# Performance work log

Hardware: AMD Instinct MI355X
Metric: run time of the kernel (lower is better)

## Reference

```python
import jax, jax.numpy as jnp
import numpy as np

DIM = 384
HEADS = 6
K = 10          # default k of DynamicGraphAttention
HID = 1536      # int(dim * mlp_ratio)
LN_EPS = 1e-5


def layernorm(x, g, b):
    m = jnp.mean(x, -1, keepdims=True)
    var = jnp.mean((x - m) ** 2, -1, keepdims=True)
    return (x - m) * jax.lax.rsqrt(var + LN_EPS) * g + b


def setup_inputs() -> dict:
    key = jax.random.key(0)
    ks = jax.random.split(key, 12)
    B, N, M, C = 16, 1024, 512, DIM
    s = 0.02
    return dict(
        q=jax.random.normal(ks[0], (B, N, C), jnp.float32),
        v=jax.random.normal(ks[1], (B, M, C), jnp.float32),
        q_pos=jax.random.normal(ks[2], (B, N, 3), jnp.float32),
        v_pos=jax.random.normal(ks[3], (B, M, 3), jnp.float32),
        norm1_g=jnp.ones((C,), jnp.float32), norm1_b=jnp.zeros((C,), jnp.float32),
        qkv_w=jax.random.normal(ks[4], (C, 3 * C), jnp.float32) * s,  # qkv_bias=False
        proj_w=jax.random.normal(ks[5], (C, C), jnp.float32) * s,
        proj_b=jnp.zeros((C,), jnp.float32),
        normq_g=jnp.ones((C,), jnp.float32), normq_b=jnp.zeros((C,), jnp.float32),
        normv_g=jnp.ones((C,), jnp.float32), normv_b=jnp.zeros((C,), jnp.float32),
        knn_w=jax.random.normal(ks[6], (2 * C, C), jnp.float32) * s,
        knn_b=jnp.zeros((C,), jnp.float32),
        norm2_g=jnp.ones((C,), jnp.float32), norm2_b=jnp.zeros((C,), jnp.float32),
        fc1_w=jax.random.normal(ks[7], (C, HID), jnp.float32) * s,
        fc1_b=jnp.zeros((HID,), jnp.float32),
        fc2_w=jax.random.normal(ks[8], (HID, C), jnp.float32) * s,
        fc2_b=jnp.zeros((C,), jnp.float32),
    )


def reference(q, v, q_pos, v_pos,
              norm1_g, norm1_b, qkv_w, proj_w, proj_b,
              normq_g, normq_b, normv_g, normv_b, knn_w, knn_b,
              norm2_g, norm2_b, fc1_w, fc1_b, fc2_w, fc2_b):
    B, N, C = q.shape
    D = C // HEADS

    # --- multi-head self-attention with pre-norm residual ---
    x = layernorm(q, norm1_g, norm1_b)
    qkv = (x @ qkv_w).reshape(B, N, 3, HEADS, D)
    qh, kh, vh = qkv[:, :, 0], qkv[:, :, 1], qkv[:, :, 2]   # [B,N,H,D]
    attn = jnp.einsum('bnhd,bmhd->bhnm', qh, kh) * (D ** -0.5)
    attn = jax.nn.softmax(attn, axis=-1)
    sa = jnp.einsum('bhnm,bmhd->bnhd', attn, vh).reshape(B, N, C)
    sa = sa @ proj_w + proj_b
    q = q + sa

    # --- dynamic graph cross-attention (knn gather + diff-concat MLP + max) ---
    nq = layernorm(q, normq_g, normq_b)          # [B,N,C]
    nv = layernorm(v, normv_g, normv_b)          # [B,M,C]
    # squared distances between query and kv positions: [B,N,M]
    d = (jnp.sum(q_pos ** 2, -1)[:, :, None]
         + jnp.sum(v_pos ** 2, -1)[:, None, :]
         - 2.0 * jnp.einsum('bnc,bmc->bnm', q_pos, v_pos))
    _, idx = jax.lax.top_k(-d, K)                # K nearest neighbors, [B,N,K]
    local_v = jax.vmap(lambda vv, ii: vv[ii])(nv, idx)   # [B,N,K,C]
    qe = nq[:, :, None, :]                                # [B,N,1,C]
    feat = jnp.concatenate(
        [local_v - qe, jnp.broadcast_to(qe, local_v.shape)], axis=-1)  # [B,N,K,2C]
    g = jax.nn.leaky_relu(feat @ knn_w + knn_b, negative_slope=0.2)
    q = q + jnp.max(g, axis=-2)                  # max over K neighbors

    # --- MLP with pre-norm residual ---
    h = layernorm(q, norm2_g, norm2_b)
    h = jax.nn.gelu(h @ fc1_w + fc1_b, approximate=False)
    h = h @ fc2_w + fc2_b
    return q + h
```

## Files before the change

### kernel.cpp

```cpp
#include <hip/hip_runtime.h>
#include <hip/hip_bf16.h>

#define CDIM 384
#define NHEAD 6
#define DHEAD 64
#define BB 16
#define NQ 1024
#define MV 512
#define HIDD 1536
#define KNN 10

typedef __attribute__((ext_vector_type(8))) __bf16 bf16x8;
typedef __attribute__((ext_vector_type(4))) float f32x4;
typedef __attribute__((ext_vector_type(4))) short short4v;

__global__ void cast_all_kernel(const float* __restrict__ qkv_w, const float* __restrict__ proj_w,
                                const float* __restrict__ knn_w, const float* __restrict__ fc1_w,
                                const float* __restrict__ fc2_w,
                                __hip_bfloat16* __restrict__ Wqkv_t,
                                __hip_bfloat16* __restrict__ Wproj_t,
                                __hip_bfloat16* __restrict__ W1_t,
                                __hip_bfloat16* __restrict__ Wd_t,
                                __hip_bfloat16* __restrict__ Wfc1_t,
                                __hip_bfloat16* __restrict__ Wfc2_t) {
  __shared__ float t1[32][33];
  __shared__ float t2[32][33];
  int gid = blockIdx.x;
  int tx = threadIdx.x, ty = threadIdx.y;
  if (gid >= 576 && gid < 720) {
    int id = gid - 576;
    int k0 = (id % 12) * 32, n0 = (id / 12) * 32;
#pragma unroll
    for (int i = 0; i < 4; i++) {
      int k = k0 + ty + i * 8;
      float w1 = knn_w[(size_t)k * CDIM + n0 + tx];
      float w2 = knn_w[(size_t)(CDIM + k) * CDIM + n0 + tx];
      t1[ty + i * 8][tx] = w1;
      t2[ty + i * 8][tx] = w2 - w1;
    }
    __syncthreads();
#pragma unroll
    for (int i = 0; i < 4; i++) {
      W1_t[(size_t)(n0 + ty + i * 8) * CDIM + k0 + tx] = __float2bfloat16(t1[tx][ty + i * 8]);
      Wd_t[(size_t)(n0 + ty + i * 8) * CDIM + k0 + tx] = __float2bfloat16(t2[tx][ty + i * 8]);
    }
    return;
  }
  const float* W;
  __hip_bfloat16* Wt;
  int Kd, Nd, k0, n0;
  if (gid < 432) {
    W = qkv_w; Wt = Wqkv_t; Kd = 384; Nd = 1152;
    k0 = (gid % 12) * 32; n0 = (gid / 12) * 32;
  } else if (gid < 576) {
    int id = gid - 432;
    W = proj_w; Wt = Wproj_t; Kd = 384; Nd = 384;
    k0 = (id % 12) * 32; n0 = (id / 12) * 32;
  } else if (gid < 1296) {
    int id = gid - 720;
    W = fc1_w; Wt = Wfc1_t; Kd = 384; Nd = 1536;
    k0 = (id % 12) * 32; n0 = (id / 12) * 32;
  } else {
    int id = gid - 1296;
    W = fc2_w; Wt = Wfc2_t; Kd = 1536; Nd = 384;
    k0 = (id % 48) * 32; n0 = (id / 48) * 32;
  }
#pragma unroll
  for (int i = 0; i < 4; i++)
    t1[ty + i * 8][tx] = W[(size_t)(k0 + ty + i * 8) * Nd + n0 + tx];
  __syncthreads();
#pragma unroll
  for (int i = 0; i < 4; i++)
    Wt[(size_t)(n0 + ty + i * 8) * Kd + k0 + tx] = __float2bfloat16(t1[tx][ty + i * 8]);
}

__device__ inline void ln_row(const float* __restrict__ xr, const float* __restrict__ gw,
                              const float* __restrict__ bw, __hip_bfloat16* __restrict__ outr,
                              int lane) {
  float v0[6];
  float s = 0.f;
#pragma unroll
  for (int i = 0; i < 3; i++) {
    float2 t = *reinterpret_cast<const float2*>(xr + i * 128 + lane * 2);
    v0[i * 2] = t.x; v0[i * 2 + 1] = t.y; s += t.x + t.y;
  }
  for (int off = 32; off; off >>= 1) s += __shfl_xor(s, off);
  float mean = s * (1.f / 384.f);
  float sq = 0.f;
#pragma unroll
  for (int i = 0; i < 6; i++) { float d = v0[i] - mean; sq += d * d; }
  for (int off = 32; off; off >>= 1) sq += __shfl_xor(sq, off);
  float rstd = rsqrtf(sq * (1.f / 384.f) + 1e-5f);
#pragma unroll
  for (int i = 0; i < 3; i++) {
    int c = i * 128 + lane * 2;
    float2 gg = *reinterpret_cast<const float2*>(gw + c);
    float2 bb = *reinterpret_cast<const float2*>(bw + c);
    __hip_bfloat162 p;
    p.x = __float2bfloat16((v0[i * 2] - mean) * rstd * gg.x + bb.x);
    p.y = __float2bfloat16((v0[i * 2 + 1] - mean) * rstd * gg.y + bb.y);
    *reinterpret_cast<__hip_bfloat162*>(outr + c) = p;
  }
}

__global__ __launch_bounds__(256) void ln_kernel(const float* __restrict__ x,
                                                 const float* __restrict__ gw,
                                                 const float* __restrict__ bw,
                                                 __hip_bfloat16* __restrict__ out, int rows) {
  int wave = (int)((blockIdx.x * blockDim.x + threadIdx.x) >> 6);
  int lane = threadIdx.x & 63;
  if (wave >= rows) return;
  ln_row(x + (size_t)wave * CDIM, gw, bw, out + (size_t)wave * CDIM, lane);
}

__global__ __launch_bounds__(256) void ln_dual_kernel(const float* __restrict__ q1,
                                                      const float* __restrict__ v,
                                                      const float* __restrict__ gq,
                                                      const float* __restrict__ bq,
                                                      const float* __restrict__ gv,
                                                      const float* __restrict__ bv,
                                                      __hip_bfloat16* __restrict__ Xbf,
                                                      __hip_bfloat16* __restrict__ NV) {
  int wave = (int)((blockIdx.x * blockDim.x + threadIdx.x) >> 6);
  int lane = threadIdx.x & 63;
  if (wave < BB * NQ) {
    ln_row(q1 + (size_t)wave * CDIM, gq, bq, Xbf + (size_t)wave * CDIM, lane);
  } else {
    int r = wave - BB * NQ;
    ln_row(v + (size_t)r * CDIM, gv, bv, NV + (size_t)r * CDIM, lane);
  }
}

template <int EPI>
__global__ __launch_bounds__(256) void gemm_kernel(const __hip_bfloat16* __restrict__ A,
                                                   const __hip_bfloat16* __restrict__ Bt,
                                                   const float* __restrict__ bias,
                                                   const float* __restrict__ resid,
                                                   void* __restrict__ outp,
                                                   void* __restrict__ out2,
                                                   void* __restrict__ out3,
                                                   int M, int N, int Kdim) {
  __shared__ __align__(16) __hip_bfloat16 As[128 * 64];
  __shared__ __align__(16) __hip_bfloat16 Bs[128 * 64];
  int m0 = blockIdx.y * 128, n0 = blockIdx.x * 128;
  int t = threadIdx.x;
  int lane = t & 63, w = t >> 6;
  int wrow = w >> 1, wcol = w & 1;
  int lg = lane >> 4, lr = lane & 15;
  int gcol = (((lane & 7) ^ (lane >> 3)) * 8);
  const __hip_bfloat16* Ab = A + (size_t)(m0 + w * 8 + (lane >> 3)) * Kdim + gcol;
  const __hip_bfloat16* Bb = Bt + (size_t)(n0 + w * 8 + (lane >> 3)) * Kdim + gcol;
  char* AsB = (char*)As;
  char* BsB = (char*)Bs;
  f32x4 acc[4][4] = {};
  for (int k0 = 0; k0 < Kdim; k0 += 64) {
    if (k0) __syncthreads();
#pragma unroll
    for (int i = 0; i < 4; i++)
      __builtin_amdgcn_global_load_lds(
          (const __attribute__((address_space(1))) void*)(Ab + (size_t)(i * 32) * Kdim + k0),
          (__attribute__((address_space(3))) void*)(AsB + (i * 4 + w) * 1024), 16, 0, 0);
#pragma unroll
    for (int i = 0; i < 4; i++)
      __builtin_amdgcn_global_load_lds(
          (const __attribute__((address_space(1))) void*)(Bb + (size_t)(i * 32) * Kdim + k0),
          (__attribute__((address_space(3))) void*)(BsB + (i * 4 + w) * 1024), 16, 0, 0);
    __syncthreads();
#pragma unroll
    for (int kk = 0; kk < 2; kk++) {
      bf16x8 a[4], b[4];
#pragma unroll
      for (int i = 0; i < 4; i++) {
        int ra = wrow * 64 + i * 16 + lr;
        int rb = wcol * 64 + i * 16 + lr;
        int sw = (((kk << 2) | lg) ^ (lr & 7)) * 16;
        a[i] = *reinterpret_cast<const bf16x8*>(AsB + ra * 128 + sw);
        b[i] = *reinterpret_cast<const bf16x8*>(BsB + rb * 128 + sw);
      }
#pragma unroll
      for (int i = 0; i < 4; i++)
#pragma unroll
        for (int j = 0; j < 4; j++)
          acc[i][j] = __builtin_amdgcn_mfma_f32_16x16x32_bf16(a[i], b[j], acc[i][j], 0, 0, 0);
    }
  }
#pragma unroll
  for (int i = 0; i < 4; i++)
#pragma unroll
    for (int j = 0; j < 4; j++) {
      int col = n0 + wcol * 64 + j * 16 + lr;
#pragma unroll
      for (int r = 0; r < 4; r++) {
        int row = m0 + wrow * 64 + i * 16 + lg * 4 + r;
        float v = acc[i][j][r];
        if (EPI == 5) {
          int b = row >> 10, n = row & 1023;
          if (col < CDIM) {
            int h = col >> 6, d = col & 63;
            ((__hip_bfloat16*)outp)[(((size_t)(b * NHEAD + h)) * NQ + n) * DHEAD + d] =
                __float2bfloat16(v * 0.18033688f);
          } else if (col < 2 * CDIM) {
            int c = col - CDIM, h = c >> 6, d = c & 63;
            ((__hip_bfloat16*)out2)[(((size_t)(b * NHEAD + h)) * NQ + n) * DHEAD + d] =
                __float2bfloat16(v);
          } else {
            int c = col - 2 * CDIM, h = c >> 6, d = c & 63;
            ((__hip_bfloat16*)out3)[(((size_t)(b * NHEAD + h)) * DHEAD + d) * NQ + n] =
                __float2bfloat16(v);
          }
        } else {
          if (EPI == 1 || EPI == 2 || EPI == 3) v += bias[col];
          if (EPI == 2) v += resid[(size_t)row * N + col];
          if (EPI == 3) v = 0.5f * v * (1.f + erff(v * 0.70710678118654752f));
          if (EPI == 0 || EPI == 3)
            ((__hip_bfloat16*)outp)[(size_t)row * N + col] = __float2bfloat16(v);
          else
            ((float*)outp)[(size_t)row * N + col] = v;
        }
      }
    }
}

__global__ __launch_bounds__(256) void attn_kernel(const __hip_bfloat16* __restrict__ Qb,
                                                   const __hip_bfloat16* __restrict__ Kb,
                                                   const __hip_bfloat16* __restrict__ Vt,
                                                   __hip_bfloat16* __restrict__ SAb) {
  __shared__ __align__(16) __hip_bfloat16 Ks[2][64][72];
  __shared__ __align__(16) __hip_bfloat16 Vs[2][64][72];
  int bh = blockIdx.x % 96;
  int qblk = blockIdx.x / 96;
  int t = threadIdx.x;
  int w = t >> 6, lane = t & 63;
  int lg = lane >> 4, lr = lane & 15;
  const __hip_bfloat16* Qp = Qb + (size_t)bh * NQ * DHEAD;
  const __hip_bfloat16* Kp = Kb + (size_t)bh * NQ * DHEAD;
  const __hip_bfloat16* Vp = Vt + (size_t)bh * DHEAD * NQ;
  int q0 = qblk * 128 + w * 32;
  bf16x8 qf[2][2];
#pragma unroll
  for (int qt = 0; qt < 2; qt++)
#pragma unroll
    for (int kk = 0; kk < 2; kk++)
      qf[qt][kk] = *reinterpret_cast<const bf16x8*>(
          Qp + (size_t)(q0 + qt * 16 + lr) * DHEAD + kk * 32 + lg * 8);
  int srow = w * 16 + (lane >> 2);
  int scol = (lane & 3) * 16;
  uint4 kr0 = *reinterpret_cast<const uint4*>(Kp + (size_t)srow * DHEAD + scol);
  uint4 kr1 = *reinterpret_cast<const uint4*>(Kp + (size_t)srow * DHEAD + scol + 8);
  uint4 vr0 = *reinterpret_cast<const uint4*>(Vp + (size_t)srow * NQ + scol);
  uint4 vr1 = *reinterpret_cast<const uint4*>(Vp + (size_t)srow * NQ + scol + 8);
  *reinterpret_cast<uint4*>(&Ks[0][srow][scol]) = kr0;
  *reinterpret_cast<uint4*>(&Ks[0][srow][scol + 8]) = kr1;
  *reinterpret_cast<uint4*>(&Vs[0][srow][scol]) = vr0;
  *reinterpret_cast<uint4*>(&Vs[0][srow][scol + 8]) = vr1;
  f32x4 o[2][4] = {};
  float m_[2] = {-1e30f, -1e30f};
  float l_[2] = {0.f, 0.f};
  __syncthreads();
  for (int kt = 0; kt < 16; kt++) {
    int cur = kt & 1;
    if (kt < 15) {
      int kb = (kt + 1) * 64;
      kr0 = *reinterpret_cast<const uint4*>(Kp + (size_t)(kb + srow) * DHEAD + scol);
      kr1 = *reinterpret_cast<const uint4*>(Kp + (size_t)(kb + srow) * DHEAD + scol + 8);
      vr0 = *reinterpret_cast<const uint4*>(Vp + (size_t)srow * NQ + kb + scol);
      vr1 = *reinterpret_cast<const uint4*>(Vp + (size_t)srow * NQ + kb + scol + 8);
    }
    f32x4 s[4][2] = {};
#pragma unroll
    for (int kti = 0; kti < 4; kti++)
#pragma unroll
      for (int kk = 0; kk < 2; kk++) {
        bf16x8 a = *reinterpret_cast<const bf16x8*>(&Ks[cur][kti * 16 + lr][kk * 32 + lg * 8]);
#pragma unroll
        for (int qt = 0; qt < 2; qt++)
          s[kti][qt] = __builtin_amdgcn_mfma_f32_16x16x32_bf16(a, qf[qt][kk], s[kti][qt], 0, 0, 0);
      }
#pragma unroll
    for (int qt = 0; qt < 2; qt++) {
      float a0 = fmaxf(fmaxf(s[0][qt][0], s[0][qt][1]), fmaxf(s[0][qt][2], s[0][qt][3]));
      float a1 = fmaxf(fmaxf(s[1][qt][0], s[1][qt][1]), fmaxf(s[1][qt][2], s[1][qt][3]));
      float a2 = fmaxf(fmaxf(s[2][qt][0], s[2][qt][1]), fmaxf(s[2][qt][2], s[2][qt][3]));
      float a3 = fmaxf(fmaxf(s[3][qt][0], s[3][qt][1]), fmaxf(s[3][qt][2], s[3][qt][3]));
      float lmax = fmaxf(fmaxf(a0, a1), fmaxf(a2, a3));
      if (!__all(lmax - m_[qt] <= 8.f)) {
        float pmax = fmaxf(lmax, __shfl_xor(lmax, 16));
        pmax = fmaxf(pmax, __shfl_xor(pmax, 32));
        float mn = fmaxf(m_[qt], pmax);
        float corr = __builtin_amdgcn_exp2f(m_[qt] - mn);
        l_[qt] *= corr;
        m_[qt] = mn;
#pragma unroll
        for (int r = 0; r < 4; r++) {
          float cr = __shfl(corr, (lane & 48) | (((lane >> 4) & 3) * 4 + r));
#pragma unroll
          for (int dt = 0; dt < 4; dt++) o[qt][dt][r] *= cr;
        }
      }
      float m = m_[qt];
      float ls = 0.f;
#pragma unroll
      for (int kti = 0; kti < 4; kti++) {
        float p0 = __builtin_amdgcn_exp2f(s[kti][qt][0] - m);
        float p1 = __builtin_amdgcn_exp2f(s[kti][qt][1] - m);
        float p2 = __builtin_amdgcn_exp2f(s[kti][qt][2] - m);
        float p3 = __builtin_amdgcn_exp2f(s[kti][qt][3] - m);
        s[kti][qt][0] = p0; s[kti][qt][1] = p1; s[kti][qt][2] = p2; s[kti][qt][3] = p3;
        ls += (p0 + p1) + (p2 + p3);
      }
      l_[qt] += ls;
    }
#pragma unroll
    for (int kti = 0; kti < 4; kti++) {
      short4v pa[2];
#pragma unroll
      for (int qt = 0; qt < 2; qt++) {
#pragma unroll
        for (int r = 0; r < 4; r++) {
          __bf16 hv = (__bf16)s[kti][qt][r];
          pa[qt][r] = __builtin_bit_cast(short, hv);
        }
      }
#pragma unroll
      for (int dt = 0; dt < 4; dt++) {
        short4v vb = *reinterpret_cast<const short4v*>(&Vs[cur][dt * 16 + lr][kti * 16 + lg * 4]);
#pragma unroll
        for (int qt = 0; qt < 2; qt++)
          o[qt][dt] = __builtin_amdgcn_mfma_f32_16x16x16bf16_1k(pa[qt], vb, o[qt][dt], 0, 0, 0);
      }
    }
    if (kt < 15) {
      int nb = cur ^ 1;
      *reinterpret_cast<uint4*>(&Ks[nb][srow][scol]) = kr0;
      *reinterpret_cast<uint4*>(&Ks[nb][srow][scol + 8]) = kr1;
      *reinterpret_cast<uint4*>(&Vs[nb][srow][scol]) = vr0;
      *reinterpret_cast<uint4*>(&Vs[nb][srow][scol + 8]) = vr1;
      __syncthreads();
    }
  }
#pragma unroll
  for (int qt = 0; qt < 2; qt++) {
    l_[qt] += __shfl_xor(l_[qt], 16);
    l_[qt] += __shfl_xor(l_[qt], 32);
  }
  int b = bh / NHEAD, h = bh % NHEAD;
#pragma unroll
  for (int qt = 0; qt < 2; qt++)
#pragma unroll
    for (int r = 0; r < 4; r++) {
      float li = __shfl(l_[qt], (lane & 48) | (((lane >> 4) & 3) * 4 + r));
      float inv = 1.f / li;
      int row = q0 + qt * 16 + ((lane >> 4) & 3) * 4 + r;
#pragma unroll
      for (int dt = 0; dt < 4; dt++)
        SAb[((size_t)(b * NQ + row)) * CDIM + h * DHEAD + dt * 16 + lr] =
            __float2bfloat16(o[qt][dt][r] * inv);
    }
}

__global__ __launch_bounds__(256) void knn_fused_kernel(const float* __restrict__ q_pos,
                                                        const float* __restrict__ v_pos,
                                                        const float* __restrict__ A1,
                                                        const float* __restrict__ A2,
                                                        const float* __restrict__ q1,
                                                        const float* __restrict__ g2,
                                                        const float* __restrict__ b2,
                                                        float* __restrict__ q2,
                                                        __hip_bfloat16* __restrict__ xout) {
  int wq = (int)((blockIdx.x * blockDim.x + threadIdx.x) >> 6);
  int lane = threadIdx.x & 63;
  if (wq >= BB * NQ) return;
  int b = wq >> 10;
  const float* qp = q_pos + (size_t)wq * 3;
  double qx = qp[0], qy = qp[1], qz = qp[2];
  double qs = qx * qx + qy * qy + qz * qz;
  double dloc[8];
#pragma unroll
  for (int j = 0; j < 8; j++) {
    int m = lane + 64 * j;
    const float* vp = v_pos + ((size_t)b * MV + m) * 3;
    double vx = vp[0], vy = vp[1], vz = vp[2];
    double vs = vx * vx + vy * vy + vz * vz;
    dloc[j] = qs + vs - 2.0 * (qx * vx + qy * vy + qz * vz);
  }
  float a2[6], mx[6];
#pragma unroll
  for (int i = 0; i < 6; i++) {
    a2[i] = A2[(size_t)wq * CDIM + lane + 64 * i];
    mx[i] = -1e30f;
  }
  for (int k = 0; k < KNN; k++) {
    double best = dloc[0];
    int bj = 0;
#pragma unroll
    for (int j = 1; j < 8; j++)
      if (dloc[j] < best) { best = dloc[j]; bj = j; }
    int bm = lane + 64 * bj;
    for (int off = 1; off < 64; off <<= 1) {
      double od = __shfl_xor(best, off);
      int om = __shfl_xor(bm, off);
      if (od < best || (od == best && om < bm)) { best = od; bm = om; }
    }
    const float* a1 = A1 + ((size_t)b * MV + bm) * CDIM;
#pragma unroll
    for (int i = 0; i < 6; i++) {
      float g = a1[lane + 64 * i] + a2[i];
      g = g > 0.f ? g : 0.2f * g;
      mx[i] = fmaxf(mx[i], g);
    }
#pragma unroll
    for (int j = 0; j < 8; j++)
      if (bm == lane + 64 * j) dloc[j] = 1e300;
  }
  float vals[6];
  float s = 0.f;
#pragma unroll
  for (int i = 0; i < 6; i++) {
    vals[i] = q1[(size_t)wq * CDIM + lane + 64 * i] + mx[i];
    s += vals[i];
  }
  for (int off = 32; off; off >>= 1) s += __shfl_xor(s, off);
  float mean = s * (1.f / 384.f);
  float sq = 0.f;
#pragma unroll
  for (int i = 0; i < 6; i++) { float d = vals[i] - mean; sq += d * d; }
  for (int off = 32; off; off >>= 1) sq += __shfl_xor(sq, off);
  float rstd = rsqrtf(sq * (1.f / 384.f) + 1e-5f);
#pragma unroll
  for (int i = 0; i < 6; i++) {
    int c = lane + 64 * i;
    q2[(size_t)wq * CDIM + c] = vals[i];
    xout[(size_t)wq * CDIM + c] = __float2bfloat16((vals[i] - mean) * rstd * g2[c] + b2[c]);
  }
}

extern "C" void kernel_launch(void* const* d_in, const int* in_sizes, int n_in,
                              void* d_out, int out_size, void* d_ws, size_t ws_size,
                              hipStream_t stream) {
  const float* q = (const float*)d_in[0];
  const float* v = (const float*)d_in[1];
  const float* q_pos = (const float*)d_in[2];
  const float* v_pos = (const float*)d_in[3];
  const float* norm1_g = (const float*)d_in[4];
  const float* norm1_b = (const float*)d_in[5];
  const float* qkv_w = (const float*)d_in[6];
  const float* proj_w = (const float*)d_in[7];
  const float* proj_b = (const float*)d_in[8];
  const float* normq_g = (const float*)d_in[9];
  const float* normq_b = (const float*)d_in[10];
  const float* normv_g = (const float*)d_in[11];
  const float* normv_b = (const float*)d_in[12];
  const float* knn_w = (const float*)d_in[13];
  const float* knn_b = (const float*)d_in[14];
  const float* norm2_g = (const float*)d_in[15];
  const float* norm2_b = (const float*)d_in[16];
  const float* fc1_w = (const float*)d_in[17];
  const float* fc1_b = (const float*)d_in[18];
  const float* fc2_w = (const float*)d_in[19];
  const float* fc2_b = (const float*)d_in[20];

  char* ws = (char*)d_ws;
  const size_t SZ_Wqkv = (size_t)1152 * 384 * 2;
  const size_t SZ_W384 = (size_t)384 * 384 * 2;
  const size_t SZ_Wfc = (size_t)1536 * 384 * 2;
  const size_t SZ_Xbf = (size_t)16384 * 384 * 2;
  const size_t SZ_QKV = (size_t)16384 * 1152 * 2;
  const size_t SZ_q32 = (size_t)16384 * 384 * 4;
  const size_t SZ_NV = (size_t)8192 * 384 * 2;

  size_t o_Wqkv = 0;
  size_t o_Wproj = o_Wqkv + SZ_Wqkv;
  size_t o_W1 = o_Wproj + SZ_W384;
  size_t o_Wd = o_W1 + SZ_W384;
  size_t o_Wfc1 = o_Wd + SZ_W384;
  size_t o_Wfc2 = o_Wfc1 + SZ_Wfc;
  size_t o_Xbf = o_Wfc2 + SZ_Wfc;
  size_t o_QKV = o_Xbf + SZ_Xbf;
  size_t o_A1 = o_QKV;
  size_t o_A2 = o_QKV + (size_t)8192 * 384 * 4;
  size_t o_Qb = o_QKV + SZ_QKV;
  size_t o_Kb = o_Qb + SZ_Xbf;
  size_t o_Vt = o_Kb + SZ_Xbf;
  size_t o_SA = o_Vt + SZ_Xbf;
  size_t o_H1 = o_Qb;
  size_t o_q1 = o_SA + SZ_Xbf;
  size_t o_NV = o_q1 + SZ_q32;
  size_t o_q2 = o_NV + SZ_NV;

  __hip_bfloat16* Wqkv_t = (__hip_bfloat16*)(ws + o_Wqkv);
  __hip_bfloat16* Wproj_t = (__hip_bfloat16*)(ws + o_Wproj);
  __hip_bfloat16* W1_t = (__hip_bfloat16*)(ws + o_W1);
  __hip_bfloat16* Wd_t = (__hip_bfloat16*)(ws + o_Wd);
  __hip_bfloat16* Wfc1_t = (__hip_bfloat16*)(ws + o_Wfc1);
  __hip_bfloat16* Wfc2_t = (__hip_bfloat16*)(ws + o_Wfc2);
  __hip_bfloat16* Xbf = (__hip_bfloat16*)(ws + o_Xbf);
  float* A1f = (float*)(ws + o_A1);
  float* A2f = (float*)(ws + o_A2);
  __hip_bfloat16* Qb = (__hip_bfloat16*)(ws + o_Qb);
  __hip_bfloat16* Kb = (__hip_bfloat16*)(ws + o_Kb);
  __hip_bfloat16* Vt = (__hip_bfloat16*)(ws + o_Vt);
  __hip_bfloat16* SAb = (__hip_bfloat16*)(ws + o_SA);
  __hip_bfloat16* H1 = (__hip_bfloat16*)(ws + o_H1);
  float* q1 = (float*)(ws + o_q1);
  __hip_bfloat16* NV = (__hip_bfloat16*)(ws + o_NV);
  float* q2 = (float*)(ws + o_q2);
  float* outf = (float*)d_out;

  cast_all_kernel<<<1872, dim3(32, 8), 0, stream>>>(qkv_w, proj_w, knn_w, fc1_w, fc2_w,
                                                    Wqkv_t, Wproj_t, W1_t, Wd_t, Wfc1_t, Wfc2_t);
  ln_kernel<<<4096, 256, 0, stream>>>(q, norm1_g, norm1_b, Xbf, 16384);
  gemm_kernel<5><<<dim3(9, 128), 256, 0, stream>>>(Xbf, Wqkv_t, nullptr, nullptr,
                                                   Qb, Kb, Vt, 16384, 1152, 384);
  attn_kernel<<<768, 256, 0, stream>>>(Qb, Kb, Vt, SAb);
  gemm_kernel<2><<<dim3(3, 128), 256, 0, stream>>>(SAb, Wproj_t, proj_b, q, q1,
                                                   nullptr, nullptr, 16384, 384, 384);
  ln_dual_kernel<<<6144, 256, 0, stream>>>(q1, v, normq_g, normq_b, normv_g, normv_b, Xbf, NV);
  gemm_kernel<4><<<dim3(3, 64), 256, 0, stream>>>(NV, W1_t, nullptr, nullptr, A1f,
                                                  nullptr, nullptr, 8192, 384, 384);
  gemm_kernel<1><<<dim3(3, 128), 256, 0, stream>>>(Xbf, Wd_t, knn_b, nullptr, A2f,
                                                   nullptr, nullptr, 16384, 384, 384);
  knn_fused_kernel<<<4096, 256, 0, stream>>>(q_pos, v_pos, A1f, A2f, q1,
                                             norm2_g, norm2_b, q2, Xbf);
  gemm_kernel<3><<<dim3(12, 128), 256, 0, stream>>>(Xbf, Wfc1_t, fc1_b, nullptr, H1,
                                                    nullptr, nullptr, 16384, 1536, 384);
  gemm_kernel<2><<<dim3(3, 128), 256, 0, stream>>>(H1, Wfc2_t, fc2_b, q2, outf,
                                                   nullptr, nullptr, 16384, 384, 1536);
}
```

Before: 335.1 us.

## Merge weight cast with LN1, batch KNN GEMMs, use 64-row tiles for N=384 GEMMs

Folds the weight transpose/cast and the first layernorm into one prep kernel, and merges the two KNN projection GEMMs (A1 from NV, A2 from normalized q) into a single launch. The GEMM is templated on M tile size, and the N=384 GEMMs now use 64-row tiles. On a 256-CU part this doubles the block count from 384 to 768, which should fill the GPU better. The trade-off is less A/B reuse per block, and W1_t and Wd_t must sit contiguously in the workspace.

```diff
diff --git a/kernel.cpp b/kernel.cpp
--- a/kernel.cpp
+++ b/kernel.cpp
@@ -14,19 +14,54 @@
 typedef __attribute__((ext_vector_type(4))) float f32x4;
 typedef __attribute__((ext_vector_type(4))) short short4v;
 
-__global__ void cast_all_kernel(const float* __restrict__ qkv_w, const float* __restrict__ proj_w,
-                                const float* __restrict__ knn_w, const float* __restrict__ fc1_w,
-                                const float* __restrict__ fc2_w,
-                                __hip_bfloat16* __restrict__ Wqkv_t,
-                                __hip_bfloat16* __restrict__ Wproj_t,
-                                __hip_bfloat16* __restrict__ W1_t,
-                                __hip_bfloat16* __restrict__ Wd_t,
-                                __hip_bfloat16* __restrict__ Wfc1_t,
-                                __hip_bfloat16* __restrict__ Wfc2_t) {
+__device__ inline void ln_row(const float* __restrict__ xr, const float* __restrict__ gw,
+                              const float* __restrict__ bw, __hip_bfloat16* __restrict__ outr,
+                              int lane) {
+  float v0[6];
+  float s = 0.f;
+#pragma unroll
+  for (int i = 0; i < 3; i++) {
+    float2 t = *reinterpret_cast<const float2*>(xr + i * 128 + lane * 2);
+    v0[i * 2] = t.x; v0[i * 2 + 1] = t.y; s += t.x + t.y;
+  }
+  for (int off = 32; off; off >>= 1) s += __shfl_xor(s, off);
+  float mean = s * (1.f / 384.f);
+  float sq = 0.f;
+#pragma unroll
+  for (int i = 0; i < 6; i++) { float d = v0[i] - mean; sq += d * d; }
+  for (int off = 32; off; off >>= 1) sq += __shfl_xor(sq, off);
+  float rstd = rsqrtf(sq * (1.f / 384.f) + 1e-5f);
+#pragma unroll
+  for (int i = 0; i < 3; i++) {
+    int c = i * 128 + lane * 2;
+    float2 gg = *reinterpret_cast<const float2*>(gw + c);
+    float2 bb = *reinterpret_cast<const float2*>(bw + c);
+    __hip_bfloat162 p;
+    p.x = __float2bfloat16((v0[i * 2] - mean) * rstd * gg.x + bb.x);
+    p.y = __float2bfloat16((v0[i * 2 + 1] - mean) * rstd * gg.y + bb.y);
+    *reinterpret_cast<__hip_bfloat162*>(outr + c) = p;
+  }
+}
+
+__global__ __launch_bounds__(256) void prep_kernel(
+    const float* __restrict__ qkv_w, const float* __restrict__ proj_w,
+    const float* __restrict__ knn_w, const float* __restrict__ fc1_w,
+    const float* __restrict__ fc2_w, const float* __restrict__ q,
+    const float* __restrict__ g1, const float* __restrict__ b1,
+    __hip_bfloat16* __restrict__ Wqkv_t, __hip_bfloat16* __restrict__ Wproj_t,
+    __hip_bfloat16* __restrict__ W1_t, __hip_bfloat16* __restrict__ Wd_t,
+    __hip_bfloat16* __restrict__ Wfc1_t, __hip_bfloat16* __restrict__ Wfc2_t,
+    __hip_bfloat16* __restrict__ Xbf) {
+  int gid = blockIdx.x;
+  if (gid >= 1872) {
+    int wave = (gid - 1872) * 4 + ((int)threadIdx.x >> 6);
+    int lane = threadIdx.x & 63;
+    ln_row(q + (size_t)wave * CDIM, g1, b1, Xbf + (size_t)wave * CDIM, lane);
+    return;
+  }
   __shared__ float t1[32][33];
   __shared__ float t2[32][33];
-  int gid = blockIdx.x;
-  int tx = threadIdx.x, ty = threadIdx.y;
+  int tx = threadIdx.x & 31, ty = (int)threadIdx.x >> 5;
   if (gid >= 576 && gid < 720) {
     int id = gid - 576;
     int k0 = (id % 12) * 32, n0 = (id / 12) * 32;
@@ -74,45 +109,6 @@
     Wt[(size_t)(n0 + ty + i * 8) * Kd + k0 + tx] = __float2bfloat16(t1[tx][ty + i * 8]);
 }
 
-__device__ inline void ln_row(const float* __restrict__ xr, const float* __restrict__ gw,
-                              const float* __restrict__ bw, __hip_bfloat16* __restrict__ outr,
-                              int lane) {
-  float v0[6];
-  float s = 0.f;
-#pragma unroll
-  for (int i = 0; i < 3; i++) {
-    float2 t = *reinterpret_cast<const float2*>(xr + i * 128 + lane * 2);
-    v0[i * 2] = t.x; v0[i * 2 + 1] = t.y; s += t.x + t.y;
-  }
-  for (int off = 32; off; off >>= 1) s += __shfl_xor(s, off);
-  float mean = s * (1.f / 384.f);
-  float sq = 0.f;
-#pragma unroll
-  for (int i = 0; i < 6; i++) { float d = v0[i] - mean; sq += d * d; }
-  for (int off = 32; off; off >>= 1) sq += __shfl_xor(sq, off);
-  float rstd = rsqrtf(sq * (1.f / 384.f) + 1e-5f);
-#pragma unroll
-  for (int i = 0; i < 3; i++) {
-    int c = i * 128 + lane * 2;
-    float2 gg = *reinterpret_cast<const float2*>(gw + c);
-    float2 bb = *reinterpret_cast<const float2*>(bw + c);
-    __hip_bfloat162 p;
-    p.x = __float2bfloat16((v0[i * 2] - mean) * rstd * gg.x + bb.x);
-    p.y = __float2bfloat16((v0[i * 2 + 1] - mean) * rstd * gg.y + bb.y);
-    *reinterpret_cast<__hip_bfloat162*>(outr + c) = p;
-  }
-}
-
-__global__ __launch_bounds__(256) void ln_kernel(const float* __restrict__ x,
-                                                 const float* __restrict__ gw,
-                                                 const float* __restrict__ bw,
-                                                 __hip_bfloat16* __restrict__ out, int rows) {
-  int wave = (int)((blockIdx.x * blockDim.x + threadIdx.x) >> 6);
-  int lane = threadIdx.x & 63;
-  if (wave >= rows) return;
-  ln_row(x + (size_t)wave * CDIM, gw, bw, out + (size_t)wave * CDIM, lane);
-}
-
 __global__ __launch_bounds__(256) void ln_dual_kernel(const float* __restrict__ q1,
                                                       const float* __restrict__ v,
                                                       const float* __restrict__ gq,
@@ -131,7 +127,7 @@
   }
 }
 
-template <int EPI>
+template <int EPI, int BM>
 __global__ __launch_bounds__(256) void gemm_kernel(const __hip_bfloat16* __restrict__ A,
                                                    const __hip_bfloat16* __restrict__ Bt,
                                                    const float* __restrict__ bias,
@@ -140,23 +136,37 @@
                                                    void* __restrict__ out2,
                                                    void* __restrict__ out3,
                                                    int M, int N, int Kdim) {
-  __shared__ __align__(16) __hip_bfloat16 As[128 * 64];
+  constexpr int MI = BM / 32;
+  __shared__ __align__(16) __hip_bfloat16 As[BM * 64];
   __shared__ __align__(16) __hip_bfloat16 Bs[128 * 64];
-  int m0 = blockIdx.y * 128, n0 = blockIdx.x * 128;
+  int m0 = blockIdx.y * BM, n0 = blockIdx.x * 128;
+  const __hip_bfloat16* Ause = A;
+  const __hip_bfloat16* Bt_use = Bt;
+  bool isA1 = false;
+  if (EPI == 6) {
+    constexpr int A2B = 16384 / BM;
+    if ((int)blockIdx.y >= A2B) {
+      isA1 = true;
+      m0 = (blockIdx.y - A2B) * BM;
+      Ause = (const __hip_bfloat16*)out3;
+    } else {
+      Bt_use = Bt + (size_t)384 * 384;
+    }
+  }
   int t = threadIdx.x;
   int lane = t & 63, w = t >> 6;
   int wrow = w >> 1, wcol = w & 1;
   int lg = lane >> 4, lr = lane & 15;
   int gcol = (((lane & 7) ^ (lane >> 3)) * 8);
-  const __hip_bfloat16* Ab = A + (size_t)(m0 + w * 8 + (lane >> 3)) * Kdim + gcol;
-  const __hip_bfloat16* Bb = Bt + (size_t)(n0 + w * 8 + (lane >> 3)) * Kdim + gcol;
+  const __hip_bfloat16* Ab = Ause + (size_t)(m0 + w * 8 + (lane >> 3)) * Kdim + gcol;
+  const __hip_bfloat16* Bb = Bt_use + (size_t)(n0 + w * 8 + (lane >> 3)) * Kdim + gcol;
   char* AsB = (char*)As;
   char* BsB = (char*)Bs;
-  f32x4 acc[4][4] = {};
+  f32x4 acc[MI][4] = {};
   for (int k0 = 0; k0 < Kdim; k0 += 64) {
     if (k0) __syncthreads();
 #pragma unroll
-    for (int i = 0; i < 4; i++)
+    for (int i = 0; i < MI; i++)
       __builtin_amdgcn_global_load_lds(
           (const __attribute__((address_space(1))) void*)(Ab + (size_t)(i * 32) * Kdim + k0),
           (__attribute__((address_space(3))) void*)(AsB + (i * 4 + w) * 1024), 16, 0, 0);
@@ -168,30 +178,34 @@
     __syncthreads();
 #pragma unroll
     for (int kk = 0; kk < 2; kk++) {
-      bf16x8 a[4], b[4];
-#pragma unroll
-      for (int i = 0; i < 4; i++) {
-        int ra = wrow * 64 + i * 16 + lr;
-        int rb = wcol * 64 + i * 16 + lr;
+      bf16x8 a[MI], b[4];
+#pragma unroll
+      for (int i = 0; i < MI; i++) {
+        int ra = wrow * (BM / 2) + i * 16 + lr;
         int sw = (((kk << 2) | lg) ^ (lr & 7)) * 16;
         a[i] = *reinterpret_cast<const bf16x8*>(AsB + ra * 128 + sw);
-        b[i] = *reinterpret_cast<const bf16x8*>(BsB + rb * 128 + sw);
-      }
-#pragma unroll
-      for (int i = 0; i < 4; i++)
+      }
+#pragma unroll
+      for (int j = 0; j < 4; j++) {
+        int rb = wcol * 64 + j * 16 + lr;
+        int sw = (((kk << 2) | lg) ^ (lr & 7)) * 16;
+        b[j] = *reinterpret_cast<const bf16x8*>(BsB + rb * 128 + sw);
+      }
+#pragma unroll
+      for (int i = 0; i < MI; i++)
 #pragma unroll
         for (int j = 0; j < 4; j++)
           acc[i][j] = __builtin_amdgcn_mfma_f32_16x16x32_bf16(a[i], b[j], acc[i][j], 0, 0, 0);
     }
   }
 #pragma unroll
-  for (int i = 0; i < 4; i++)
+  for (int i = 0; i < MI; i++)
 #pragma unroll
     for (int j = 0; j < 4; j++) {
       int col = n0 + wcol * 64 + j * 16 + lr;
 #pragma unroll
       for (int r = 0; r < 4; r++) {
-        int row = m0 + wrow * 64 + i * 16 + lg * 4 + r;
+        int row = m0 + wrow * (BM / 2) + i * 16 + lg * 4 + r;
         float v = acc[i][j][r];
         if (EPI == 5) {
           int b = row >> 10, n = row & 1023;
@@ -208,6 +222,11 @@
             ((__hip_bfloat16*)out3)[(((size_t)(b * NHEAD + h)) * DHEAD + d) * NQ + n] =
                 __float2bfloat16(v);
           }
+        } else if (EPI == 6) {
+          float vv = v;
+          if (!isA1) vv += bias[col];
+          float* dst = isA1 ? (float*)out2 : (float*)outp;
+          dst[(size_t)row * 384 + col] = vv;
         } else {
           if (EPI == 1 || EPI == 2 || EPI == 3) v += bias[col];
           if (EPI == 2) v += resid[(size_t)row * N + col];
@@ -506,23 +525,21 @@
   float* q2 = (float*)(ws + o_q2);
   float* outf = (float*)d_out;
 
-  cast_all_kernel<<<1872, dim3(32, 8), 0, stream>>>(qkv_w, proj_w, knn_w, fc1_w, fc2_w,
-                                                    Wqkv_t, Wproj_t, W1_t, Wd_t, Wfc1_t, Wfc2_t);
-  ln_kernel<<<4096, 256, 0, stream>>>(q, norm1_g, norm1_b, Xbf, 16384);
-  gemm_kernel<5><<<dim3(9, 128), 256, 0, stream>>>(Xbf, Wqkv_t, nullptr, nullptr,
-                                                   Qb, Kb, Vt, 16384, 1152, 384);
+  prep_kernel<<<5968, 256, 0, stream>>>(qkv_w, proj_w, knn_w, fc1_w, fc2_w, q,
+                                        norm1_g, norm1_b,
+                                        Wqkv_t, Wproj_t, W1_t, Wd_t, Wfc1_t, Wfc2_t, Xbf);
+  gemm_kernel<5, 128><<<dim3(9, 128), 256, 0, stream>>>(Xbf, Wqkv_t, nullptr, nullptr,
+                                                        Qb, Kb, Vt, 16384, 1152, 384);
   attn_kernel<<<768, 256, 0, stream>>>(Qb, Kb, Vt, SAb);
-  gemm_kernel<2><<<dim3(3, 128), 256, 0, stream>>>(SAb, Wproj_t, proj_b, q, q1,
-                                                   nullptr, nullptr, 16384, 384, 384);
+  gemm_kernel<2, 64><<<dim3(3, 256), 256, 0, stream>>>(SAb, Wproj_t, proj_b, q, q1,
+                                                       nullptr, nullptr, 16384, 384, 384);
   ln_dual_kernel<<<6144, 256, 0, stream>>>(q1, v, normq_g, normq_b, normv_g, normv_b, Xbf, NV);
-  gemm_kernel<4><<<dim3(3, 64), 256, 0, stream>>>(NV, W1_t, nullptr, nullptr, A1f,
-                                                  nullptr, nullptr, 8192, 384, 384);
-  gemm_kernel<1><<<dim3(3, 128), 256, 0, stream>>>(Xbf, Wd_t, knn_b, nullptr, A2f,
-                                                   nullptr, nullptr, 16384, 384, 384);
+  gemm_kernel<6, 64><<<dim3(3, 384), 256, 0, stream>>>(Xbf, W1_t, knn_b, nullptr, A2f,
+                                                       A1f, (void*)NV, 16384, 384, 384);
   knn_fused_kernel<<<4096, 256, 0, stream>>>(q_pos, v_pos, A1f, A2f, q1,
                                              norm2_g, norm2_b, q2, Xbf);
-  gemm_kernel<3><<<dim3(12, 128), 256, 0, stream>>>(Xbf, Wfc1_t, fc1_b, nullptr, H1,
-                                                    nullptr, nullptr, 16384, 1536, 384);
-  gemm_kernel<2><<<dim3(3, 128), 256, 0, stream>>>(H1, Wfc2_t, fc2_b, q2, outf,
-                                                   nullptr, nullptr, 16384, 384, 1536);
-}
+  gemm_kernel<3, 128><<<dim3(12, 128), 256, 0, stream>>>(Xbf, Wfc1_t, fc1_b, nullptr, H1,
+                                                         nullptr, nullptr, 16384, 1536, 384);
+  gemm_kernel<2, 64><<<dim3(3, 256), 256, 0, stream>>>(H1, Wfc2_t, fc2_b, q2, outf,
+                                                       nullptr, nullptr, 16384, 384, 1536);
+}
```

Measured after the change: 305.9 us. 8.7% less time.
